# Kernel tuning notes

Hardware: AMD Instinct MI355X
Metric: run time of the kernel (lower is better)

## Reference

```python
import jax, jax.numpy as jnp
import numpy as np

NEG_SLOPE = 0.2   # PyG GATConv default negative_slope
LN_EPS = 1e-5
SOFTMAX_EPS = 1e-16  # PyG softmax denominator eps


def setup_inputs() -> dict:
    key = jax.random.key(0)
    ks = jax.random.split(key, 6)
    N, IN, OUT, H, E = 100000, 128, 64, 2, 1600000
    X = jax.random.normal(ks[0], (N, IN), dtype=jnp.float32)
    edge_index = jax.random.randint(ks[1], (2, E), 0, N, dtype=jnp.int64)
    W = jax.random.normal(ks[2], (H * OUT, IN), dtype=jnp.float32) * 0.05
    att_src = jax.random.normal(ks[3], (H, OUT), dtype=jnp.float32) * 0.05
    att_dst = jax.random.normal(ks[4], (H, OUT), dtype=jnp.float32) * 0.05
    bias = jnp.zeros((OUT,), dtype=jnp.float32)
    ln_gamma = jnp.ones((OUT,), dtype=jnp.float32)
    ln_beta = jnp.zeros((OUT,), dtype=jnp.float32)
    return {"X": X, "edge_index": edge_index, "W": W, "att_src": att_src,
            "att_dst": att_dst, "bias": bias, "ln_gamma": ln_gamma, "ln_beta": ln_beta}


def reference(X, edge_index, W, att_src, att_dst, bias, ln_gamma, ln_beta):
    N = X.shape[0]
    H, F = att_src.shape
    # PyG GATConv default: add self-loops
    loops = jnp.arange(N, dtype=edge_index.dtype)
    src = jnp.concatenate([edge_index[0], loops])  # [Et]
    dst = jnp.concatenate([edge_index[1], loops])  # [Et]
    # linear projection: x' = X @ W^T  -> [N, H, F]
    x = (X @ W.T).reshape(N, H, F)
    # per-node attention logits  [N, H]
    a_src = jnp.einsum('nhf,hf->nh', x, att_src)
    a_dst = jnp.einsum('nhf,hf->nh', x, att_dst)
    # per-edge logits, leaky relu  [Et, H]
    e = jax.nn.leaky_relu(a_src[src] + a_dst[dst], NEG_SLOPE)
    # segment softmax over incoming edges of each dst node
    m = jax.ops.segment_max(e, dst, num_segments=N)          # [N, H]
    ex = jnp.exp(e - m[dst])
    denom = jax.ops.segment_sum(ex, dst, num_segments=N)     # [N, H]
    alpha = ex / (denom[dst] + SOFTMAX_EPS)                  # [Et, H]
    # weighted scatter-add of source features
    msg = x[src] * alpha[:, :, None]                         # [Et, H, F]
    out = jax.ops.segment_sum(msg, dst, num_segments=N)      # [N, H, F]
    # concat=False -> mean over heads, then bias
    out = out.mean(axis=1) + bias                            # [N, F]
    # LayerNorm over features
    mu = out.mean(axis=-1, keepdims=True)
    var = ((out - mu) ** 2).mean(axis=-1, keepdims=True)
    h = (out - mu) * jax.lax.rsqrt(var + LN_EPS) * ln_gamma + ln_beta
    return h
```

## Files before the change

kernel.cpp:

```cpp
#include <hip/hip_runtime.h>
#include <hip/hip_bf16.h>

#define NEG_SLOPE 0.2f
#define LN_EPS 1e-5f
#define SM_EPS 1e-16f

typedef __attribute__((ext_vector_type(8))) short bf16x8;
typedef __attribute__((ext_vector_type(4))) float f32x4;

__device__ inline unsigned short f2bf(float f) {
    unsigned u = __float_as_uint(f);
    return (unsigned short)((u + 0x7FFFu + ((u >> 16) & 1u)) >> 16);
}
__device__ inline float bf_lo(unsigned int v) { return __uint_as_float(v << 16); }
__device__ inline float bf_hi(unsigned int v) { return __uint_as_float(v & 0xffff0000u); }

#define NBIN 512
#define BCAP 4864
#define SCHUNK 4096
#define CURPAD 16

__global__ __launch_bounds__(256) void k_gs(const float* __restrict__ X,
                                            const float* __restrict__ W,
                                            const float* __restrict__ att_src,
                                            const float* __restrict__ att_dst,
                                            unsigned int* __restrict__ xp,
                                            float4* __restrict__ PS,
                                            float4* __restrict__ PD,
                                            const int* __restrict__ ei,
                                            int* __restrict__ binCursor,
                                            unsigned int* __restrict__ tmp,
                                            int N, int E, int SB) {
    __shared__ __align__(16) char smem[52224];
    const int t = threadIdx.x;

    if ((int)blockIdx.x < SB) {
        int* off = (int*)smem;
        const int base = blockIdx.x * SCHUNK;

        int bn[16];
        unsigned int pe[16];
#pragma unroll
        for (int k = 0; k < 16; ++k) {
            int i = base + k * 256 + t;
            if (i < E) {
                int s = ei[i];
                int d = ei[E + i];
                bn[k] = d >> 8;
                pe[k] = ((unsigned)(d & 255) << 24) | (unsigned)s;
            } else {
                bn[k] = -1;
            }
        }

        for (int i = t; i < NBIN; i += 256) off[i] = 0;
        __syncthreads();
#pragma unroll
        for (int k = 0; k < 16; ++k)
            if (bn[k] >= 0) atomicAdd(&off[bn[k]], 1);
        __syncthreads();
        for (int i = t; i < NBIN; i += 256) {
            int h = off[i];
            off[i] = h ? (atomicAdd(&binCursor[i * CURPAD], h) + i * BCAP) : 0;
        }
        __syncthreads();
#pragma unroll
        for (int k = 0; k < 16; ++k) {
            if (bn[k] >= 0) {
                int p = atomicAdd(&off[bn[k]], 1);
                tmp[p] = pe[k];
            }
        }
        return;
    }

    unsigned short* Ws = (unsigned short*)smem;
    unsigned short* Xs = (unsigned short*)(smem + 34816);
    const int b0 = ((int)blockIdx.x - SB) * 64;
    const int lane = t & 63;
    const int w = t >> 6;
    const int c15 = lane & 15;
    const int quad = lane >> 4;

#pragma unroll
    for (int i = 0; i < 16; ++i) {
        int f = i * 256 + t;
        int nr = f >> 5;
        int q = f & 31;
        float4 v = reinterpret_cast<const float4*>(W)[nr * 32 + q];
        ushort4 b;
        b.x = f2bf(v.x); b.y = f2bf(v.y); b.z = f2bf(v.z); b.w = f2bf(v.w);
        *reinterpret_cast<ushort4*>(&Ws[nr * 136 + q * 4]) = b;
    }
#pragma unroll
    for (int i = 0; i < 8; ++i) {
        int f = i * 256 + t;
        int m = f >> 5;
        int q = f & 31;
        int gr = b0 + m;
        if (gr >= N) gr = N - 1;
        float4 v = reinterpret_cast<const float4*>(X)[(size_t)gr * 32 + q];
        ushort4 b;
        b.x = f2bf(v.x); b.y = f2bf(v.y); b.z = f2bf(v.z); b.w = f2bf(v.w);
        *reinterpret_cast<ushort4*>(&Xs[m * 136 + q * 4]) = b;
    }
    __syncthreads();

    f32x4 acc[8];
#pragma unroll
    for (int ct = 0; ct < 8; ++ct) acc[ct] = (f32x4){0.f, 0.f, 0.f, 0.f};

#pragma unroll
    for (int kc = 0; kc < 4; ++kc) {
        bf16x8 af = *reinterpret_cast<const bf16x8*>(
            &Xs[(w * 16 + c15) * 136 + kc * 32 + quad * 8]);
#pragma unroll
        for (int ct = 0; ct < 8; ++ct) {
            bf16x8 bfr = *reinterpret_cast<const bf16x8*>(
                &Ws[(ct * 16 + c15) * 136 + kc * 32 + quad * 8]);
            acc[ct] = __builtin_amdgcn_mfma_f32_16x16x32_bf16(af, bfr, acc[ct], 0, 0, 0);
        }
    }

    float attS[8], attD[8];
#pragma unroll
    for (int ct = 0; ct < 8; ++ct) {
        attS[ct] = att_src[ct * 16 + c15];
        attD[ct] = att_dst[ct * 16 + c15];
    }

#pragma unroll
    for (int r = 0; r < 4; ++r) {
        int row = b0 + w * 16 + quad * 4 + r;
        float s0 = 0.f, s1 = 0.f, d0 = 0.f, d1 = 0.f;
#pragma unroll
        for (int ct = 0; ct < 4; ++ct) {
            s0 += acc[ct][r] * attS[ct];
            d0 += acc[ct][r] * attD[ct];
            s1 += acc[ct + 4][r] * attS[ct + 4];
            d1 += acc[ct + 4][r] * attD[ct + 4];
        }
#pragma unroll
        for (int o = 1; o < 16; o <<= 1) {
            s0 += __shfl_xor(s0, o);
            s1 += __shfl_xor(s1, o);
            d0 += __shfl_xor(d0, o);
            d1 += __shfl_xor(d1, o);
        }
        if (row < N) {
#pragma unroll
            for (int ct = 0; ct < 4; ++ct) {
                unsigned int p = (unsigned int)f2bf(acc[ct][r]) |
                                 ((unsigned int)f2bf(acc[ct + 4][r]) << 16);
                xp[(size_t)row * 64 + ct * 16 + c15] = p;
            }
            if (c15 == 0) {
                PS[row] = make_float4(__expf(s0), __expf(NEG_SLOPE * s0),
                                      __expf(s1), __expf(NEG_SLOPE * s1));
                PD[row] = make_float4(__expf(d0), __expf(NEG_SLOPE * d0),
                                      __expf(d1), __expf(NEG_SLOPE * d1));
            }
        }
    }
}

__global__ __launch_bounds__(1024) void k_bucket(const unsigned int* __restrict__ tmp,
                                                 const int* __restrict__ binCursor,
                                                 const float4* __restrict__ PS,
                                                 const float4* __restrict__ PD,
                                                 uint2* __restrict__ csr,
                                                 unsigned int* __restrict__ rowPtr,
                                                 float4* __restrict__ metaN,
                                                 int N) {
    __shared__ int cnt[256];
    __shared__ int cur[256];
    __shared__ int lds[4];
    __shared__ float den0[256], den1[256];
    __shared__ float4 pdc[256];
    const int t = threadIdx.x;
    const int b = blockIdx.x;
    const int start = b * BCAP;
    const int d0 = b * 256;
    int m = binCursor[b * CURPAD];
    if (m > BCAP) m = BCAP;

    if (t < 256) {
        cnt[t] = 0; den0[t] = 0.f; den1[t] = 0.f;
        int d = d0 + t;
        pdc[t] = (d < N) ? PD[d] : make_float4(0.f, 0.f, 0.f, 0.f);
    }
    __syncthreads();

    unsigned int ee[5], uu[5];
#pragma unroll
    for (int it = 0; it < 5; ++it) {
        int k = t + it * 1024;
        ee[it] = 0xFFFFFFFFu;
        if (k < m) {
            unsigned int e = tmp[start + k];
            ee[it] = e;
            int li = e >> 24;
            int s = (int)(e & 0x00FFFFFFu);
            float4 ps = PS[s];
            float4 pd = pdc[li];
            float m0 = ps.x * pd.x, mp0 = ps.y * pd.y;
            float m1 = ps.z * pd.z, mp1 = ps.w * pd.w;
            float u0 = (m0 >= 1.f) ? m0 : mp0;
            float u1 = (m1 >= 1.f) ? m1 : mp1;
            unsigned int u01;
            asm("v_cvt_pk_bf16_f32 %0, %1, %2" : "=v"(u01) : "v"(u0), "v"(u1));
            uu[it] = u01;
            atomicAdd(&cnt[li], 1);
            atomicAdd(&den0[li], bf_lo(u01));
            atomicAdd(&den1[li], bf_hi(u01));
        }
    }
    __syncthreads();

    const int lane = t & 63, w = t >> 6;
    int v = 0, incl = 0;
    if (t < 256) {
        v = cnt[t];
        incl = v;
#pragma unroll
        for (int o = 1; o < 64; o <<= 1) {
            int u = __shfl_up(incl, o);
            if (lane >= o) incl += u;
        }
        if (lane == 63) lds[w] = incl;
    }
    __syncthreads();
    if (t == 0) {
        int run = 0;
        for (int i = 0; i < 4; ++i) { int tv = lds[i]; lds[i] = run; run += tv; }
    }
    __syncthreads();
    if (t < 256) {
        int excl = lds[w] + incl - v;
        cur[t] = excl;
        int d = d0 + t;
        if (d < N) {
            rowPtr[d] = (unsigned)(start + excl) | ((unsigned)v << 22);
            float4 ps = PS[d];
            float4 pd = pdc[t];
            float sm0 = ps.x * pd.x, smp0 = ps.y * pd.y;
            float sm1 = ps.z * pd.z, smp1 = ps.w * pd.w;
            float us0 = (sm0 >= 1.f) ? sm0 : smp0;
            float us1 = (sm1 >= 1.f) ? sm1 : smp1;
            float D0 = den0[t] + us0, D1 = den1[t] + us1;
            metaN[d] = make_float4(us0, us1,
                                   0.5f / (D0 + SM_EPS), 0.5f / (D1 + SM_EPS));
        }
    }
    __syncthreads();

#pragma unroll
    for (int it = 0; it < 5; ++it) {
        if (ee[it] != 0xFFFFFFFFu) {
            int li = ee[it] >> 24;
            int p = atomicAdd(&cur[li], 1);
            csr[start + p] = make_uint2(ee[it] & 0x00FFFFFFu, uu[it]);
        }
    }
}

__global__ __launch_bounds__(256) void k_agg(const unsigned int* __restrict__ xp,
                                             const float4* __restrict__ metaN,
                                             const unsigned int* __restrict__ rowPtr,
                                             const uint2* __restrict__ csr,
                                             const float* __restrict__ bias,
                                             const float* __restrict__ gamma,
                                             const float* __restrict__ beta,
                                             float* __restrict__ out, int N) {
    const int w = threadIdx.x >> 6, lane = threadIdx.x & 63;
    const int n = blockIdx.x * 4 + w;
    if (n >= N) return;

    float4 meta = metaN[n];
    unsigned int vself = xp[((unsigned)n << 6) | lane];
    float S0 = meta.x * bf_lo(vself);
    float S1 = meta.y * bf_hi(vself);

    unsigned int pr = rowPtr[n];
    const int jb = (int)(pr & 0x3FFFFFu);
    const int je = jb + (int)(pr >> 22);
    int j = jb;
    const int nfull = (je - jb) >> 3;

    uint2 cc[8];
    if (nfull > 0) {
        int ju = __builtin_amdgcn_readfirstlane(j);
#pragma unroll
        for (int q = 0; q < 8; ++q) cc[q] = csr[ju + q];
    }
    for (int bI = 0; bI < nfull; ++bI) {
        unsigned int v[8];
#pragma unroll
        for (int q = 0; q < 8; ++q) v[q] = xp[(cc[q].x << 6) | lane];
        uint2 cn[8];
        {
            int jn = (bI + 1 < nfull) ? (j + 8) : jb;
            int ju = __builtin_amdgcn_readfirstlane(jn);
#pragma unroll
            for (int q = 0; q < 8; ++q) cn[q] = csr[ju + q];
        }
#pragma unroll
        for (int q = 0; q < 8; ++q) {
            S0 = fmaf(bf_lo(cc[q].y), bf_lo(v[q]), S0);
            S1 = fmaf(bf_hi(cc[q].y), bf_hi(v[q]), S1);
        }
#pragma unroll
        for (int q = 0; q < 8; ++q) cc[q] = cn[q];
        j += 8;
    }
    for (; j + 3 < je; j += 4) {
        int ju = __builtin_amdgcn_readfirstlane(j);
        uint2 c[4];
#pragma unroll
        for (int q = 0; q < 4; ++q) c[q] = csr[ju + q];
        unsigned int v[4];
#pragma unroll
        for (int q = 0; q < 4; ++q) v[q] = xp[(c[q].x << 6) | lane];
#pragma unroll
        for (int q = 0; q < 4; ++q) {
            S0 = fmaf(bf_lo(c[q].y), bf_lo(v[q]), S0);
            S1 = fmaf(bf_hi(c[q].y), bf_hi(v[q]), S1);
        }
    }
    for (; j < je; ++j) {
        uint2 c = csr[__builtin_amdgcn_readfirstlane(j)];
        unsigned int vv = xp[(c.x << 6) | lane];
        S0 = fmaf(bf_lo(c.y), bf_lo(vv), S0);
        S1 = fmaf(bf_hi(c.y), bf_hi(vv), S1);
    }

    float o = meta.z * S0 + meta.w * S1 + bias[lane];

    float mu = o;
#pragma unroll
    for (int d = 32; d > 0; d >>= 1) mu += __shfl_xor(mu, d);
    mu *= (1.0f / 64.0f);
    float dv = o - mu;
    float var = dv * dv;
#pragma unroll
    for (int d = 32; d > 0; d >>= 1) var += __shfl_xor(var, d);
    var *= (1.0f / 64.0f);
    out[(size_t)n * 64 + lane] = dv * rsqrtf(var + LN_EPS) * gamma[lane] + beta[lane];
}

extern "C" void kernel_launch(void* const* d_in, const int* in_sizes, int n_in,
                              void* d_out, int out_size, void* d_ws, size_t ws_size,
                              hipStream_t stream) {
    const float* X        = (const float*)d_in[0];
    const int*   ei       = (const int*)d_in[1];
    const float* W        = (const float*)d_in[2];
    const float* att_src  = (const float*)d_in[3];
    const float* att_dst  = (const float*)d_in[4];
    const float* bias     = (const float*)d_in[5];
    const float* ln_gamma = (const float*)d_in[6];
    const float* ln_beta  = (const float*)d_in[7];
    float* out = (float*)d_out;

    const int N = in_sizes[0] / 128;
    const int E = in_sizes[1] / 2;
    const int NBUCK = (N + 255) / 256;
    const int SB = (E + SCHUNK - 1) / SCHUNK;
    const int GB = (N + 63) / 64;

    char* ws = (char*)d_ws;
    size_t off = 0;
    auto alloc = [&](size_t bytes) {
        size_t o = off;
        off += (bytes + 255) & ~(size_t)255;
        return o;
    };
    unsigned int* xp     = (unsigned int*)(ws + alloc((size_t)N * 64 * 4));
    float4* PS           = (float4*)(ws + alloc((size_t)N * 16));
    float4* PD           = (float4*)(ws + alloc((size_t)N * 16));
    float4* metaN        = (float4*)(ws + alloc((size_t)N * 16));
    unsigned int* rowPtr = (unsigned int*)(ws + alloc((size_t)N * 4));
    uint2* csr           = (uint2*)(ws + alloc((size_t)NBIN * BCAP * 8));
    unsigned int* tmp    = (unsigned int*)(ws + alloc((size_t)NBIN * BCAP * 4));
    int* binCursor       = (int*)(ws + alloc(NBIN * CURPAD * 4));

    hipMemsetAsync(binCursor, 0, (size_t)NBIN * CURPAD * 4, stream);
    k_gs<<<SB + GB, 256, 0, stream>>>(X, W, att_src, att_dst, xp, PS, PD,
                                      ei, binCursor, tmp, N, E, SB);
    k_bucket<<<NBUCK, 1024, 0, stream>>>(tmp, binCursor, PS, PD, csr, rowPtr,
                                         metaN, N);
    k_agg<<<(N + 3) / 4, 256, 0, stream>>>(xp, metaN, rowPtr, csr,
                                           bias, ln_gamma, ln_beta, out, N);
}
```

Baseline: 229.1 us.

## Move softmax denominator into aggregation and process two nodes per wavefront

The bucket kernel no longer computes per-destination softmax denominators with LDS float atomics, drops the metaN array, and runs with 512 threads, using a two-pass loop (count, then compute and scatter). The aggregation kernel recomputes the self-loop weight from PS/PD, sums the denominator as it walks the edges, and interleaves two destination nodes per wave to expose more independent gathers. The goal is to cut LDS atomic contention and register pressure in bucketing and to raise memory-level parallelism in aggregation. The cost is padded work when the two nodes' degrees differ, clamped duplicate CSR loads, and a second read of tmp in bucketing.

```diff
diff --git a/kernel.cpp b/kernel.cpp
--- a/kernel.cpp
+++ b/kernel.cpp
@@ -164,18 +164,16 @@
     }
 }
 
-__global__ __launch_bounds__(1024) void k_bucket(const unsigned int* __restrict__ tmp,
-                                                 const int* __restrict__ binCursor,
-                                                 const float4* __restrict__ PS,
-                                                 const float4* __restrict__ PD,
-                                                 uint2* __restrict__ csr,
-                                                 unsigned int* __restrict__ rowPtr,
-                                                 float4* __restrict__ metaN,
-                                                 int N) {
+__global__ __launch_bounds__(512) void k_bucket(const unsigned int* __restrict__ tmp,
+                                                const int* __restrict__ binCursor,
+                                                const float4* __restrict__ PS,
+                                                const float4* __restrict__ PD,
+                                                uint2* __restrict__ csr,
+                                                unsigned int* __restrict__ rowPtr,
+                                                int N) {
     __shared__ int cnt[256];
     __shared__ int cur[256];
     __shared__ int lds[4];
-    __shared__ float den0[256], den1[256];
     __shared__ float4 pdc[256];
     const int t = threadIdx.x;
     const int b = blockIdx.x;
@@ -185,35 +183,14 @@
     if (m > BCAP) m = BCAP;
 
     if (t < 256) {
-        cnt[t] = 0; den0[t] = 0.f; den1[t] = 0.f;
+        cnt[t] = 0;
         int d = d0 + t;
         pdc[t] = (d < N) ? PD[d] : make_float4(0.f, 0.f, 0.f, 0.f);
     }
     __syncthreads();
 
-    unsigned int ee[5], uu[5];
-#pragma unroll
-    for (int it = 0; it < 5; ++it) {
-        int k = t + it * 1024;
-        ee[it] = 0xFFFFFFFFu;
-        if (k < m) {
-            unsigned int e = tmp[start + k];
-            ee[it] = e;
-            int li = e >> 24;
-            int s = (int)(e & 0x00FFFFFFu);
-            float4 ps = PS[s];
-            float4 pd = pdc[li];
-            float m0 = ps.x * pd.x, mp0 = ps.y * pd.y;
-            float m1 = ps.z * pd.z, mp1 = ps.w * pd.w;
-            float u0 = (m0 >= 1.f) ? m0 : mp0;
-            float u1 = (m1 >= 1.f) ? m1 : mp1;
-            unsigned int u01;
-            asm("v_cvt_pk_bf16_f32 %0, %1, %2" : "=v"(u01) : "v"(u0), "v"(u1));
-            uu[it] = u01;
-            atomicAdd(&cnt[li], 1);
-            atomicAdd(&den0[li], bf_lo(u01));
-            atomicAdd(&den1[li], bf_hi(u01));
-        }
+    for (int k = t; k < m; k += 512) {
+        atomicAdd(&cnt[tmp[start + k] >> 24], 1);
     }
     __syncthreads();
 
@@ -239,33 +216,30 @@
         int excl = lds[w] + incl - v;
         cur[t] = excl;
         int d = d0 + t;
-        if (d < N) {
-            rowPtr[d] = (unsigned)(start + excl) | ((unsigned)v << 22);
-            float4 ps = PS[d];
-            float4 pd = pdc[t];
-            float sm0 = ps.x * pd.x, smp0 = ps.y * pd.y;
-            float sm1 = ps.z * pd.z, smp1 = ps.w * pd.w;
-            float us0 = (sm0 >= 1.f) ? sm0 : smp0;
-            float us1 = (sm1 >= 1.f) ? sm1 : smp1;
-            float D0 = den0[t] + us0, D1 = den1[t] + us1;
-            metaN[d] = make_float4(us0, us1,
-                                   0.5f / (D0 + SM_EPS), 0.5f / (D1 + SM_EPS));
-        }
-    }
-    __syncthreads();
-
-#pragma unroll
-    for (int it = 0; it < 5; ++it) {
-        if (ee[it] != 0xFFFFFFFFu) {
-            int li = ee[it] >> 24;
-            int p = atomicAdd(&cur[li], 1);
-            csr[start + p] = make_uint2(ee[it] & 0x00FFFFFFu, uu[it]);
-        }
+        if (d < N) rowPtr[d] = (unsigned)(start + excl) | ((unsigned)v << 22);
+    }
+    __syncthreads();
+
+    for (int k = t; k < m; k += 512) {
+        unsigned int e = tmp[start + k];
+        int li = e >> 24;
+        int s = (int)(e & 0x00FFFFFFu);
+        float4 ps = PS[s];
+        float4 pd = pdc[li];
+        float m0 = ps.x * pd.x, mp0 = ps.y * pd.y;
+        float m1 = ps.z * pd.z, mp1 = ps.w * pd.w;
+        float u0 = (m0 >= 1.f) ? m0 : mp0;
+        float u1 = (m1 >= 1.f) ? m1 : mp1;
+        unsigned int u01;
+        asm("v_cvt_pk_bf16_f32 %0, %1, %2" : "=v"(u01) : "v"(u0), "v"(u1));
+        int p = atomicAdd(&cur[li], 1);
+        csr[start + p] = make_uint2((unsigned)s, u01);
     }
 }
 
 __global__ __launch_bounds__(256) void k_agg(const unsigned int* __restrict__ xp,
-                                             const float4* __restrict__ metaN,
+                                             const float4* __restrict__ PS,
+                                             const float4* __restrict__ PD,
                                              const unsigned int* __restrict__ rowPtr,
                                              const uint2* __restrict__ csr,
                                              const float* __restrict__ bias,
@@ -273,79 +247,117 @@
                                              const float* __restrict__ beta,
                                              float* __restrict__ out, int N) {
     const int w = threadIdx.x >> 6, lane = threadIdx.x & 63;
-    const int n = blockIdx.x * 4 + w;
-    if (n >= N) return;
-
-    float4 meta = metaN[n];
-    unsigned int vself = xp[((unsigned)n << 6) | lane];
-    float S0 = meta.x * bf_lo(vself);
-    float S1 = meta.y * bf_hi(vself);
-
-    unsigned int pr = rowPtr[n];
-    const int jb = (int)(pr & 0x3FFFFFu);
-    const int je = jb + (int)(pr >> 22);
-    int j = jb;
-    const int nfull = (je - jb) >> 3;
-
-    uint2 cc[8];
-    if (nfull > 0) {
-        int ju = __builtin_amdgcn_readfirstlane(j);
-#pragma unroll
-        for (int q = 0; q < 8; ++q) cc[q] = csr[ju + q];
-    }
-    for (int bI = 0; bI < nfull; ++bI) {
-        unsigned int v[8];
-#pragma unroll
-        for (int q = 0; q < 8; ++q) v[q] = xp[(cc[q].x << 6) | lane];
-        uint2 cn[8];
+    const int pidx = blockIdx.x * 4 + w;
+    const int n0 = pidx * 2;
+    if (n0 >= N) return;
+    const bool hasB = (n0 + 1 < N);
+    const int n1 = hasB ? n0 + 1 : n0;
+
+    float4 psA = PS[n0], pdA = PD[n0];
+    float4 psB = PS[n1], pdB = PD[n1];
+    float mA0 = psA.x * pdA.x, mpA0 = psA.y * pdA.y;
+    float mA1 = psA.z * pdA.z, mpA1 = psA.w * pdA.w;
+    float usA0 = (mA0 >= 1.f) ? mA0 : mpA0;
+    float usA1 = (mA1 >= 1.f) ? mA1 : mpA1;
+    float mB0 = psB.x * pdB.x, mpB0 = psB.y * pdB.y;
+    float mB1 = psB.z * pdB.z, mpB1 = psB.w * pdB.w;
+    float usB0 = (mB0 >= 1.f) ? mB0 : mpB0;
+    float usB1 = (mB1 >= 1.f) ? mB1 : mpB1;
+
+    unsigned int vsA = xp[((unsigned)n0 << 6) | lane];
+    unsigned int vsB = xp[((unsigned)n1 << 6) | lane];
+    float SA0 = usA0 * bf_lo(vsA), SA1 = usA1 * bf_hi(vsA);
+    float SB0 = usB0 * bf_lo(vsB), SB1 = usB1 * bf_hi(vsB);
+    float DA0 = usA0, DA1 = usA1, DB0 = usB0, DB1 = usB1;
+
+    unsigned int prA = rowPtr[n0];
+    unsigned int prB = rowPtr[n1];
+    int jA = (int)(prA & 0x3FFFFFu), degA = (int)(prA >> 22);
+    int jB = (int)(prB & 0x3FFFFFu), degB = hasB ? (int)(prB >> 22) : 0;
+    const int lastA = jA + (degA > 0 ? degA - 1 : 0);
+    const int lastB = jB + (degB > 0 ? degB - 1 : 0);
+    int remA = degA, remB = degB;
+    const int dmax = (degA > degB) ? degA : degB;
+    const int nb = (dmax + 7) >> 3;
+
+    uint2 ca[8], cb[8];
+    if (nb > 0) {
+        int juA = __builtin_amdgcn_readfirstlane(jA);
+        int juB = __builtin_amdgcn_readfirstlane(jB);
+#pragma unroll
+        for (int q = 0; q < 8; ++q) {
+            int ia = juA + q; if (ia > lastA) ia = lastA;
+            int ib = juB + q; if (ib > lastB) ib = lastB;
+            ca[q] = csr[ia];
+            cb[q] = csr[ib];
+        }
+    }
+
+    for (int bI = 0; bI < nb; ++bI) {
+        unsigned int va[8], vb[8];
+#pragma unroll
+        for (int q = 0; q < 8; ++q) {
+            va[q] = xp[(ca[q].x << 6) | lane];
+            vb[q] = xp[(cb[q].x << 6) | lane];
+        }
+        uint2 na2[8], nb2[8];
         {
-            int jn = (bI + 1 < nfull) ? (j + 8) : jb;
-            int ju = __builtin_amdgcn_readfirstlane(jn);
-#pragma unroll
-            for (int q = 0; q < 8; ++q) cn[q] = csr[ju + q];
+            int stp = (bI + 1 < nb) ? 8 : 0;
+            int juA = __builtin_amdgcn_readfirstlane(jA + stp);
+            int juB = __builtin_amdgcn_readfirstlane(jB + stp);
+#pragma unroll
+            for (int q = 0; q < 8; ++q) {
+                int ia = juA + q; if (ia > lastA) ia = lastA;
+                int ib = juB + q; if (ib > lastB) ib = lastB;
+                na2[q] = csr[ia];
+                nb2[q] = csr[ib];
+            }
         }
 #pragma unroll
         for (int q = 0; q < 8; ++q) {
-            S0 = fmaf(bf_lo(cc[q].y), bf_lo(v[q]), S0);
-            S1 = fmaf(bf_hi(cc[q].y), bf_hi(v[q]), S1);
-        }
-#pragma unroll
-        for (int q = 0; q < 8; ++q) cc[q] = cn[q];
-        j += 8;
-    }
-    for (; j + 3 < je; j += 4) {
-        int ju = __builtin_amdgcn_readfirstlane(j);
-        uint2 c[4];
-#pragma unroll
-        for (int q = 0; q < 4; ++q) c[q] = csr[ju + q];
-        unsigned int v[4];
-#pragma unroll
-        for (int q = 0; q < 4; ++q) v[q] = xp[(c[q].x << 6) | lane];
-#pragma unroll
-        for (int q = 0; q < 4; ++q) {
-            S0 = fmaf(bf_lo(c[q].y), bf_lo(v[q]), S0);
-            S1 = fmaf(bf_hi(c[q].y), bf_hi(v[q]), S1);
-        }
-    }
-    for (; j < je; ++j) {
-        uint2 c = csr[__builtin_amdgcn_readfirstlane(j)];
-        unsigned int vv = xp[(c.x << 6) | lane];
-        S0 = fmaf(bf_lo(c.y), bf_lo(vv), S0);
-        S1 = fmaf(bf_hi(c.y), bf_hi(vv), S1);
-    }
-
-    float o = meta.z * S0 + meta.w * S1 + bias[lane];
-
-    float mu = o;
+            unsigned int uya = (q < remA) ? ca[q].y : 0u;
+            unsigned int uyb = (q < remB) ? cb[q].y : 0u;
+            float wa0 = bf_lo(uya), wa1 = bf_hi(uya);
+            float wb0 = bf_lo(uyb), wb1 = bf_hi(uyb);
+            DA0 += wa0; DA1 += wa1;
+            DB0 += wb0; DB1 += wb1;
+            SA0 = fmaf(wa0, bf_lo(va[q]), SA0);
+            SA1 = fmaf(wa1, bf_hi(va[q]), SA1);
+            SB0 = fmaf(wb0, bf_lo(vb[q]), SB0);
+            SB1 = fmaf(wb1, bf_hi(vb[q]), SB1);
+        }
+#pragma unroll
+        for (int q = 0; q < 8; ++q) { ca[q] = na2[q]; cb[q] = nb2[q]; }
+        jA += 8; jB += 8; remA -= 8; remB -= 8;
+    }
+
+    float gm = gamma[lane], bt = beta[lane], bs = bias[lane];
+
+    float oA = (0.5f / (DA0 + SM_EPS)) * SA0 + (0.5f / (DA1 + SM_EPS)) * SA1 + bs;
+    float mu = oA;
 #pragma unroll
     for (int d = 32; d > 0; d >>= 1) mu += __shfl_xor(mu, d);
     mu *= (1.0f / 64.0f);
-    float dv = o - mu;
+    float dv = oA - mu;
     float var = dv * dv;
 #pragma unroll
     for (int d = 32; d > 0; d >>= 1) var += __shfl_xor(var, d);
     var *= (1.0f / 64.0f);
-    out[(size_t)n * 64 + lane] = dv * rsqrtf(var + LN_EPS) * gamma[lane] + beta[lane];
+    out[(size_t)n0 * 64 + lane] = dv * rsqrtf(var + LN_EPS) * gm + bt;
+
+    if (hasB) {
+        float oB = (0.5f / (DB0 + SM_EPS)) * SB0 + (0.5f / (DB1 + SM_EPS)) * SB1 + bs;
+        float mu2 = oB;
+#pragma unroll
+        for (int d = 32; d > 0; d >>= 1) mu2 += __shfl_xor(mu2, d);
+        mu2 *= (1.0f / 64.0f);
+        float dv2 = oB - mu2;
+        float var2 = dv2 * dv2;
+#pragma unroll
+        for (int d = 32; d > 0; d >>= 1) var2 += __shfl_xor(var2, d);
+        var2 *= (1.0f / 64.0f);
+        out[(size_t)n1 * 64 + lane] = dv2 * rsqrtf(var2 + LN_EPS) * gm + bt;
+    }
 }
 
 extern "C" void kernel_launch(void* const* d_in, const int* in_sizes, int n_in,
@@ -366,6 +378,7 @@
     const int NBUCK = (N + 255) / 256;
     const int SB = (E + SCHUNK - 1) / SCHUNK;
     const int GB = (N + 63) / 64;
+    const int NPAIR = (N + 1) / 2;
 
     char* ws = (char*)d_ws;
     size_t off = 0;
@@ -377,7 +390,6 @@
     unsigned int* xp     = (unsigned int*)(ws + alloc((size_t)N * 64 * 4));
     float4* PS           = (float4*)(ws + alloc((size_t)N * 16));
     float4* PD           = (float4*)(ws + alloc((size_t)N * 16));
-    float4* metaN        = (float4*)(ws + alloc((size_t)N * 16));
     unsigned int* rowPtr = (unsigned int*)(ws + alloc((size_t)N * 4));
     uint2* csr           = (uint2*)(ws + alloc((size_t)NBIN * BCAP * 8));
     unsigned int* tmp    = (unsigned int*)(ws + alloc((size_t)NBIN * BCAP * 4));
@@ -386,8 +398,7 @@
     hipMemsetAsync(binCursor, 0, (size_t)NBIN * CURPAD * 4, stream);
     k_gs<<<SB + GB, 256, 0, stream>>>(X, W, att_src, att_dst, xp, PS, PD,
                                       ei, binCursor, tmp, N, E, SB);
-    k_bucket<<<NBUCK, 1024, 0, stream>>>(tmp, binCursor, PS, PD, csr, rowPtr,
-                                         metaN, N);
-    k_agg<<<(N + 3) / 4, 256, 0, stream>>>(xp, metaN, rowPtr, csr,
-                                           bias, ln_gamma, ln_beta, out, N);
+    k_bucket<<<NBUCK, 512, 0, stream>>>(tmp, binCursor, PS, PD, csr, rowPtr, N);
+    k_agg<<<(NPAIR + 3) / 4, 256, 0, stream>>>(xp, PS, PD, rowPtr, csr,
+                                               bias, ln_gamma, ln_beta, out, N);
 }
```

Result: slower. 258.0 us (+12.6%).

## Move softmax denominator into aggregation kernel and shrink bucket block

Applied to the files above, without the earlier changes.

The bucket kernel no longer accumulates per-destination softmax denominators with shared-memory float atomics and no longer writes a metaN array. The aggregation kernel now recomputes the self-loop weight from PS/PD and sums the edge weights as it walks each row. The bucket kernel also drops from 1024 to 512 threads, reads tmp twice instead of keeping edges in registers, and computes the weights during the scatter pass. This removes two LDS float atomics per edge and one intermediate array, at the cost of an extra tmp read and a few extra adds per edge in the aggregation.

```diff
diff --git a/kernel.cpp b/kernel.cpp
--- a/kernel.cpp
+++ b/kernel.cpp
@@ -164,18 +164,16 @@
     }
 }
 
-__global__ __launch_bounds__(1024) void k_bucket(const unsigned int* __restrict__ tmp,
-                                                 const int* __restrict__ binCursor,
-                                                 const float4* __restrict__ PS,
-                                                 const float4* __restrict__ PD,
-                                                 uint2* __restrict__ csr,
-                                                 unsigned int* __restrict__ rowPtr,
-                                                 float4* __restrict__ metaN,
-                                                 int N) {
+__global__ __launch_bounds__(512) void k_bucket(const unsigned int* __restrict__ tmp,
+                                                const int* __restrict__ binCursor,
+                                                const float4* __restrict__ PS,
+                                                const float4* __restrict__ PD,
+                                                uint2* __restrict__ csr,
+                                                unsigned int* __restrict__ rowPtr,
+                                                int N) {
     __shared__ int cnt[256];
     __shared__ int cur[256];
     __shared__ int lds[4];
-    __shared__ float den0[256], den1[256];
     __shared__ float4 pdc[256];
     const int t = threadIdx.x;
     const int b = blockIdx.x;
@@ -185,35 +183,14 @@
     if (m > BCAP) m = BCAP;
 
     if (t < 256) {
-        cnt[t] = 0; den0[t] = 0.f; den1[t] = 0.f;
+        cnt[t] = 0;
         int d = d0 + t;
         pdc[t] = (d < N) ? PD[d] : make_float4(0.f, 0.f, 0.f, 0.f);
     }
     __syncthreads();
 
-    unsigned int ee[5], uu[5];
-#pragma unroll
-    for (int it = 0; it < 5; ++it) {
-        int k = t + it * 1024;
-        ee[it] = 0xFFFFFFFFu;
-        if (k < m) {
-            unsigned int e = tmp[start + k];
-            ee[it] = e;
-            int li = e >> 24;
-            int s = (int)(e & 0x00FFFFFFu);
-            float4 ps = PS[s];
-            float4 pd = pdc[li];
-            float m0 = ps.x * pd.x, mp0 = ps.y * pd.y;
-            float m1 = ps.z * pd.z, mp1 = ps.w * pd.w;
-            float u0 = (m0 >= 1.f) ? m0 : mp0;
-            float u1 = (m1 >= 1.f) ? m1 : mp1;
-            unsigned int u01;
-            asm("v_cvt_pk_bf16_f32 %0, %1, %2" : "=v"(u01) : "v"(u0), "v"(u1));
-            uu[it] = u01;
-            atomicAdd(&cnt[li], 1);
-            atomicAdd(&den0[li], bf_lo(u01));
-            atomicAdd(&den1[li], bf_hi(u01));
-        }
+    for (int k = t; k < m; k += 512) {
+        atomicAdd(&cnt[tmp[start + k] >> 24], 1);
     }
     __syncthreads();
 
@@ -239,33 +216,30 @@
         int excl = lds[w] + incl - v;
         cur[t] = excl;
         int d = d0 + t;
-        if (d < N) {
-            rowPtr[d] = (unsigned)(start + excl) | ((unsigned)v << 22);
-            float4 ps = PS[d];
-            float4 pd = pdc[t];
-            float sm0 = ps.x * pd.x, smp0 = ps.y * pd.y;
-            float sm1 = ps.z * pd.z, smp1 = ps.w * pd.w;
-            float us0 = (sm0 >= 1.f) ? sm0 : smp0;
-            float us1 = (sm1 >= 1.f) ? sm1 : smp1;
-            float D0 = den0[t] + us0, D1 = den1[t] + us1;
-            metaN[d] = make_float4(us0, us1,
-                                   0.5f / (D0 + SM_EPS), 0.5f / (D1 + SM_EPS));
-        }
-    }
-    __syncthreads();
-
-#pragma unroll
-    for (int it = 0; it < 5; ++it) {
-        if (ee[it] != 0xFFFFFFFFu) {
-            int li = ee[it] >> 24;
-            int p = atomicAdd(&cur[li], 1);
-            csr[start + p] = make_uint2(ee[it] & 0x00FFFFFFu, uu[it]);
-        }
+        if (d < N) rowPtr[d] = (unsigned)(start + excl) | ((unsigned)v << 22);
+    }
+    __syncthreads();
+
+    for (int k = t; k < m; k += 512) {
+        unsigned int e = tmp[start + k];
+        int li = e >> 24;
+        int s = (int)(e & 0x00FFFFFFu);
+        float4 ps = PS[s];
+        float4 pd = pdc[li];
+        float m0 = ps.x * pd.x, mp0 = ps.y * pd.y;
+        float m1 = ps.z * pd.z, mp1 = ps.w * pd.w;
+        float u0 = (m0 >= 1.f) ? m0 : mp0;
+        float u1 = (m1 >= 1.f) ? m1 : mp1;
+        unsigned int u01;
+        asm("v_cvt_pk_bf16_f32 %0, %1, %2" : "=v"(u01) : "v"(u0), "v"(u1));
+        int p = atomicAdd(&cur[li], 1);
+        csr[start + p] = make_uint2((unsigned)s, u01);
     }
 }
 
 __global__ __launch_bounds__(256) void k_agg(const unsigned int* __restrict__ xp,
-                                             const float4* __restrict__ metaN,
+                                             const float4* __restrict__ PS,
+                                             const float4* __restrict__ PD,
                                              const unsigned int* __restrict__ rowPtr,
                                              const uint2* __restrict__ csr,
                                              const float* __restrict__ bias,
@@ -276,10 +250,16 @@
     const int n = blockIdx.x * 4 + w;
     if (n >= N) return;
 
-    float4 meta = metaN[n];
+    float4 ps = PS[n], pd = PD[n];
+    float sm0 = ps.x * pd.x, smp0 = ps.y * pd.y;
+    float sm1 = ps.z * pd.z, smp1 = ps.w * pd.w;
+    float us0 = (sm0 >= 1.f) ? sm0 : smp0;
+    float us1 = (sm1 >= 1.f) ? sm1 : smp1;
+
     unsigned int vself = xp[((unsigned)n << 6) | lane];
-    float S0 = meta.x * bf_lo(vself);
-    float S1 = meta.y * bf_hi(vself);
+    float S0 = us0 * bf_lo(vself);
+    float S1 = us1 * bf_hi(vself);
+    float D0 = us0, D1 = us1;
 
     unsigned int pr = rowPtr[n];
     const int jb = (int)(pr & 0x3FFFFFu);
@@ -306,8 +286,10 @@
         }
 #pragma unroll
         for (int q = 0; q < 8; ++q) {
-            S0 = fmaf(bf_lo(cc[q].y), bf_lo(v[q]), S0);
-            S1 = fmaf(bf_hi(cc[q].y), bf_hi(v[q]), S1);
+            float w0 = bf_lo(cc[q].y), w1 = bf_hi(cc[q].y);
+            D0 += w0; D1 += w1;
+            S0 = fmaf(w0, bf_lo(v[q]), S0);
+            S1 = fmaf(w1, bf_hi(v[q]), S1);
         }
 #pragma unroll
         for (int q = 0; q < 8; ++q) cc[q] = cn[q];
@@ -323,18 +305,22 @@
         for (int q = 0; q < 4; ++q) v[q] = xp[(c[q].x << 6) | lane];
 #pragma unroll
         for (int q = 0; q < 4; ++q) {
-            S0 = fmaf(bf_lo(c[q].y), bf_lo(v[q]), S0);
-            S1 = fmaf(bf_hi(c[q].y), bf_hi(v[q]), S1);
+            float w0 = bf_lo(c[q].y), w1 = bf_hi(c[q].y);
+            D0 += w0; D1 += w1;
+            S0 = fmaf(w0, bf_lo(v[q]), S0);
+            S1 = fmaf(w1, bf_hi(v[q]), S1);
         }
     }
     for (; j < je; ++j) {
         uint2 c = csr[__builtin_amdgcn_readfirstlane(j)];
         unsigned int vv = xp[(c.x << 6) | lane];
-        S0 = fmaf(bf_lo(c.y), bf_lo(vv), S0);
-        S1 = fmaf(bf_hi(c.y), bf_hi(vv), S1);
-    }
-
-    float o = meta.z * S0 + meta.w * S1 + bias[lane];
+        float w0 = bf_lo(c.y), w1 = bf_hi(c.y);
+        D0 += w0; D1 += w1;
+        S0 = fmaf(w0, bf_lo(vv), S0);
+        S1 = fmaf(w1, bf_hi(vv), S1);
+    }
+
+    float o = (0.5f / (D0 + SM_EPS)) * S0 + (0.5f / (D1 + SM_EPS)) * S1 + bias[lane];
 
     float mu = o;
 #pragma unroll
@@ -377,7 +363,6 @@
     unsigned int* xp     = (unsigned int*)(ws + alloc((size_t)N * 64 * 4));
     float4* PS           = (float4*)(ws + alloc((size_t)N * 16));
     float4* PD           = (float4*)(ws + alloc((size_t)N * 16));
-    float4* metaN        = (float4*)(ws + alloc((size_t)N * 16));
     unsigned int* rowPtr = (unsigned int*)(ws + alloc((size_t)N * 4));
     uint2* csr           = (uint2*)(ws + alloc((size_t)NBIN * BCAP * 8));
     unsigned int* tmp    = (unsigned int*)(ws + alloc((size_t)NBIN * BCAP * 4));
@@ -386,8 +371,7 @@
     hipMemsetAsync(binCursor, 0, (size_t)NBIN * CURPAD * 4, stream);
     k_gs<<<SB + GB, 256, 0, stream>>>(X, W, att_src, att_dst, xp, PS, PD,
                                       ei, binCursor, tmp, N, E, SB);
-    k_bucket<<<NBUCK, 1024, 0, stream>>>(tmp, binCursor, PS, PD, csr, rowPtr,
-                                         metaN, N);
-    k_agg<<<(N + 3) / 4, 256, 0, stream>>>(xp, metaN, rowPtr, csr,
+    k_bucket<<<NBUCK, 512, 0, stream>>>(tmp, binCursor, PS, PD, csr, rowPtr, N);
+    k_agg<<<(N + 3) / 4, 256, 0, stream>>>(xp, PS, PD, rowPtr, csr,
                                            bias, ln_gamma, ln_beta, out, N);
 }
```

Result: faster. 222.3 us (-3.0%).
